# Kernel optimization log

Hardware: AMD Instinct MI355X
Metric: run time of the kernel (lower is better)

## Reference

```python
import jax, jax.numpy as jnp
import numpy as np

D_MODEL = 1024
NUM_HEADS = 16
HEAD_DIM = D_MODEL // NUM_HEADS


def setup_inputs() -> dict:
    key = jax.random.key(0)
    ks = jax.random.split(key, 9)
    B, S, D = 4, 2048, D_MODEL
    scale = 1.0 / np.sqrt(D)
    x = jax.random.normal(ks[0], (B, S, D), dtype=jnp.float32)
    wq = jax.random.normal(ks[1], (D, D), dtype=jnp.float32) * scale
    wk = jax.random.normal(ks[2], (D, D), dtype=jnp.float32) * scale
    wv = jax.random.normal(ks[3], (D, D), dtype=jnp.float32) * scale
    wo = jax.random.normal(ks[4], (D, D), dtype=jnp.float32) * scale
    bq = jax.random.normal(ks[5], (D,), dtype=jnp.float32) * 0.02
    bk = jax.random.normal(ks[6], (D,), dtype=jnp.float32) * 0.02
    bv = jax.random.normal(ks[7], (D,), dtype=jnp.float32) * 0.02
    bo = jax.random.normal(ks[8], (D,), dtype=jnp.float32) * 0.02
    return {"x": x, "wq": wq, "bq": bq, "wk": wk, "bk": bk,
            "wv": wv, "bv": bv, "wo": wo, "bo": bo}


def _split_heads(t):  # [B,S,D] -> [B,H,S,Dh]
    B, S, _ = t.shape
    return t.reshape(B, S, NUM_HEADS, HEAD_DIM).transpose(0, 2, 1, 3)


def reference(x, wq, bq, wk, bk, wv, bv, wo, bo):
    B, S, D = x.shape
    q = _split_heads(x @ wq + bq)  # [B,H,S,Dh]
    k = _split_heads(x @ wk + bk)
    v = _split_heads(x @ wv + bv)
    scores = jnp.einsum("bhqd,bhkd->bhqk", q, k) / jnp.sqrt(
        jnp.asarray(HEAD_DIM, dtype=x.dtype))
    causal = jnp.tril(jnp.ones((S, S), dtype=bool))  # [S,S]
    scores = jnp.where(causal, scores, jnp.finfo(scores.dtype).min)
    attn = jax.nn.softmax(scores, axis=-1)
    ctx = jnp.einsum("bhqk,bhkd->bhqd", attn, v)  # [B,H,S,Dh]
    ctx = ctx.transpose(0, 2, 1, 3).reshape(B, S, D)
    return ctx @ wo + bo
```

## Files before the change

### kernel.cpp

```cpp
#include <hip/hip_runtime.h>
#include <hip/hip_bf16.h>
#include <stdint.h>

#define DMODEL 1024
#define NH 16
#define DH 64
#define BATCH 4
#define SEQ 2048

#if __has_builtin(__builtin_amdgcn_exp2f)
#define EXP2F(x) __builtin_amdgcn_exp2f(x)
#else
#define EXP2F(x) exp2f(x)
#endif

typedef __attribute__((ext_vector_type(8))) short short8;
typedef __attribute__((ext_vector_type(4))) float f32x4;
typedef __attribute__((ext_vector_type(4))) ushort ushort4v;

__device__ __forceinline__ ushort f2bf(float f) {
    union { float f; unsigned u; } v; v.f = f;
    unsigned r = v.u + 0x7fffu + ((v.u >> 16) & 1u);
    return (ushort)(r >> 16);
}

__global__ __launch_bounds__(256) void convert_bf16(const float* __restrict__ src,
                                                    ushort* __restrict__ dst) {
    const size_t i = ((size_t)blockIdx.x * 256 + threadIdx.x) * 8;
    float4 a = *(const float4*)(src + i);
    float4 b = *(const float4*)(src + i + 4);
    short8 r;
    r[0] = (short)f2bf(a.x); r[1] = (short)f2bf(a.y);
    r[2] = (short)f2bf(a.z); r[3] = (short)f2bf(a.w);
    r[4] = (short)f2bf(b.x); r[5] = (short)f2bf(b.y);
    r[6] = (short)f2bf(b.z); r[7] = (short)f2bf(b.w);
    *(short8*)(dst + i) = r;
}

__global__ __launch_bounds__(256) void transpose_cvt_w4(
    const float* __restrict__ s0, const float* __restrict__ s1,
    const float* __restrict__ s2, const float* __restrict__ s3,
    ushort* __restrict__ d0, ushort* __restrict__ d1,
    ushort* __restrict__ d2, ushort* __restrict__ d3) {
    __shared__ ushort tile[64][65];
    const int z = blockIdx.z;
    const float* src = (z == 0) ? s0 : (z == 1) ? s1 : (z == 2) ? s2 : s3;
    ushort* dst = (z == 0) ? d0 : (z == 1) ? d1 : (z == 2) ? d2 : d3;
    const int bx = blockIdx.x * 64;
    const int by = blockIdx.y * 64;
    const int tx = threadIdx.x & 63, ty = threadIdx.x >> 6;
    #pragma unroll
    for (int i = 0; i < 64; i += 4)
        tile[ty + i][tx] = f2bf(src[(size_t)(by + ty + i) * DMODEL + bx + tx]);
    __syncthreads();
    #pragma unroll
    for (int i = 0; i < 64; i += 4)
        dst[(size_t)(bx + ty + i) * DMODEL + by + tx] = tile[tx][ty + i];
}

#define BK 64
#define NT 16

template <int MODE>
__global__ __launch_bounds__(512, 2) void gemm_tile(
    const ushort* __restrict__ A, const ushort* __restrict__ Bt,
    const float* __restrict__ b0, const float* __restrict__ b1,
    const float* __restrict__ b2,
    void* __restrict__ o0v, void* __restrict__ o1v, void* __restrict__ o2v) {
    __shared__ __align__(16) ushort lds[73728];
    const int tid  = threadIdx.x;
    const int lane = tid & 63;
    const int wv   = tid >> 6;

    const int bid = blockIdx.x;
    const int by  = 4 * (bid & 7) + ((bid >> 3) & 3);
    const int bx  = bid >> 5;
    const int mBase = by * 256, nBase = bx * 128;

    const int wm = (wv >> 1) * 64;
    const int wn = (wv & 1) * 64;
    const int frow = lane & 15;
    const int fq   = lane >> 4;
    const int r7   = frow & 7;
    const int sw0  = (fq ^ r7) << 3;
    const int sw1  = ((4 + fq) ^ r7) << 3;

    const int trow = tid >> 3;
    const int tcho = ((tid & 7) ^ (trow & 7)) * 8;
    const ushort* gA = A  + (size_t)(mBase + trow) * DMODEL + tcho;
    const ushort* gB = Bt + (size_t)(nBase + trow) * DMODEL + tcho;
    const int ldsw = wv * 512;

    f32x4 acc[4][4];
    #pragma unroll
    for (int i = 0; i < 4; ++i)
        #pragma unroll
        for (int j = 0; j < 4; ++j) acc[i][j] = (f32x4){0.f, 0.f, 0.f, 0.f};

#define STG(gp, off) __builtin_amdgcn_global_load_lds( \
    (const __attribute__((address_space(1))) void*)(gp), \
    (__attribute__((address_space(3))) void*)&lds[(off) + ldsw], 16, 0, 0)
#define STAGE_A(sb, u, h) STG(gA + (size_t)(h) * 64 * DMODEL + (u) * BK, \
                              (sb) + (h) * 4096)
#define STAGE_B(sb, u, h) STG(gB + (size_t)(h) * 64 * DMODEL + (u) * BK, \
                              (sb) + 16384 + (h) * 4096)

    STAGE_A(0, 0, 0); STAGE_A(0, 0, 1); STAGE_A(0, 0, 2); STAGE_A(0, 0, 3);
    STAGE_B(0, 0, 0); STAGE_B(0, 0, 1);
    STAGE_A(24576, 1, 0); STAGE_A(24576, 1, 1); STAGE_A(24576, 1, 2);
    STAGE_A(24576, 1, 3); STAGE_B(24576, 1, 0); STAGE_B(24576, 1, 1);
    asm volatile("s_waitcnt vmcnt(6)" ::: "memory");
    __builtin_amdgcn_s_barrier();

    int sc = 0;
    #pragma unroll 1
    for (int u = 0; u < NT; ++u) {
        const int scB = sc * 24576;
        const int sp  = (sc == 0) ? 2 : sc - 1;
        const int spB = sp * 24576;
        const ushort* bufA = &lds[scB + wm * 64];
        const ushort* bufB = &lds[scB + 16384 + wn * 64];

        short8 af[4][2], bf[2][2];

        #pragma unroll
        for (int f = 0; f < 4; ++f) {
            const int ro = (f * 16 + frow) * 64;
            af[f][0] = *(const short8*)&bufA[ro + sw0];
            af[f][1] = *(const short8*)&bufA[ro + sw1];
        }
        #pragma unroll
        for (int f2 = 0; f2 < 2; ++f2) {
            const int ro = (f2 * 16 + frow) * 64;
            bf[f2][0] = *(const short8*)&bufB[ro + sw0];
            bf[f2][1] = *(const short8*)&bufB[ro + sw1];
        }
        if (u + 2 < NT) {
            STAGE_A(spB, u + 2, 0); STAGE_A(spB, u + 2, 1); STAGE_A(spB, u + 2, 2);
        }
        __builtin_amdgcn_s_barrier();
        asm volatile("s_waitcnt lgkmcnt(0)" ::: "memory");
        __builtin_amdgcn_s_setprio(1);
        #pragma unroll
        for (int f = 0; f < 4; ++f)
            #pragma unroll
            for (int f2 = 0; f2 < 2; ++f2)
                #pragma unroll
                for (int ks = 0; ks < 2; ++ks)
                    acc[f][f2] = __builtin_amdgcn_mfma_f32_16x16x32_bf16(
                        af[f][ks], bf[f2][ks], acc[f][f2], 0, 0, 0);
        __builtin_amdgcn_s_setprio(0);
        __builtin_amdgcn_s_barrier();

        #pragma unroll
        for (int f2 = 0; f2 < 2; ++f2) {
            const int ro = (32 + f2 * 16 + frow) * 64;
            bf[f2][0] = *(const short8*)&bufB[ro + sw0];
            bf[f2][1] = *(const short8*)&bufB[ro + sw1];
        }
        if (u + 2 < NT) {
            STAGE_A(spB, u + 2, 3); STAGE_B(spB, u + 2, 0); STAGE_B(spB, u + 2, 1);
        }
        __builtin_amdgcn_s_barrier();
        asm volatile("s_waitcnt lgkmcnt(0)" ::: "memory");
        __builtin_amdgcn_s_setprio(1);
        #pragma unroll
        for (int f = 0; f < 4; ++f)
            #pragma unroll
            for (int f2 = 0; f2 < 2; ++f2)
                #pragma unroll
                for (int ks = 0; ks < 2; ++ks)
                    acc[f][2 + f2] = __builtin_amdgcn_mfma_f32_16x16x32_bf16(
                        af[f][ks], bf[f2][ks], acc[f][2 + f2], 0, 0, 0);
        __builtin_amdgcn_s_setprio(0);
        if (u + 2 < NT)       { asm volatile("s_waitcnt vmcnt(6)" ::: "memory"); }
        else if (u + 2 == NT) { asm volatile("s_waitcnt vmcnt(0)" ::: "memory"); }
        __builtin_amdgcn_s_barrier();
        sc = (sc == 2) ? 0 : sc + 1;
    }
#undef STG
#undef STAGE_A
#undef STAGE_B

    const int orow = fq * 4;
    const int ocol = frow;

    if (MODE == 1) {
        #pragma unroll
        for (int i = 0; i < 4; ++i)
            #pragma unroll
            for (int j = 0; j < 4; ++j)
                #pragma unroll
                for (int r = 0; r < 4; ++r) {
                    const int m = mBase + wm + i * 16 + orow + r;
                    const int n = nBase + wn + j * 16 + ocol;
                    ((float*)o0v)[(size_t)m * DMODEL + n] = acc[i][j][r] + b0[n];
                }
        return;
    }

    __syncthreads();
    ushort* o0 = (ushort*)o0v; ushort* o1 = (ushort*)o1v; ushort* o2 = (ushort*)o2v;
    ushort* sw = &lds[wv * 1152];
    const int mat = nBase >> 10;
    const int nb0 = (nBase & 1023) + wn;
    const int hb  = nb0 >> 6;
    const float* bp = (mat == 0) ? b0 : ((mat == 1) ? b1 : b2);
    float bj[4];
    #pragma unroll
    for (int j = 0; j < 4; ++j) bj[j] = bp[nb0 + j * 16 + ocol];
    const int mrow = mBase + wm;
    const int bbq = mrow >> 11;
    const int s0w = mrow & 2047;
    const float qscale = (mat == 0) ? 0.1803368801f : 1.0f;

    if (mat < 2) {
        ushort* obase = ((mat == 0) ? o0 : o1) +
                        ((size_t)(bbq * NH + hb) * SEQ + s0w) * DH;
        const int row = lane >> 2, cc = lane & 3;
        #pragma unroll
        for (int i = 0; i < 4; ++i) {
            #pragma unroll
            for (int j = 0; j < 4; ++j)
                #pragma unroll
                for (int r = 0; r < 4; ++r)
                    sw[(orow + r) * 72 + j * 16 + ocol] =
                        f2bf((acc[i][j][r] + bj[j]) * qscale);
            asm volatile("s_waitcnt lgkmcnt(0)" ::: "memory");
            #pragma unroll
            for (int p = 0; p < 2; ++p) {
                short8 v8 = *(const short8*)&sw[row * 72 + cc * 8 + p * 32];
                *(short8*)&obase[(size_t)(i * 16 + row) * DH + cc * 8 + p * 32] = v8;
            }
            asm volatile("s_waitcnt lgkmcnt(0)" ::: "memory");
        }
    } else {
        const int rowd = lane >> 2, scl = lane & 3;
        #pragma unroll
        for (int j = 0; j < 4; ++j) {
            #pragma unroll
            for (int ii = 0; ii < 4; ++ii)
                #pragma unroll
                for (int r = 0; r < 4; ++r)
                    sw[ocol * 72 + ii * 16 + orow + r] = f2bf(acc[ii][j][r] + bj[j]);
            asm volatile("s_waitcnt lgkmcnt(0)" ::: "memory");
            ushort* vbase = o2 + ((size_t)(bbq * NH + hb) * DH + j * 16 + rowd) * SEQ + s0w;
            #pragma unroll
            for (int p = 0; p < 2; ++p) {
                short8 v8 = *(const short8*)&sw[rowd * 72 + scl * 8 + p * 32];
                *(short8*)&vbase[scl * 8 + p * 32] = v8;
            }
            asm volatile("s_waitcnt lgkmcnt(0)" ::: "memory");
        }
    }
}

#define PSTR 72
__global__ __launch_bounds__(256, 4) void flash_attn(
    const ushort* __restrict__ Q, const ushort* __restrict__ K,
    const ushort* __restrict__ Vt, ushort* __restrict__ ctx) {
    __shared__ __align__(16) ushort Ks[4096];
    __shared__ __align__(16) ushort Vs[4096];
    __shared__ __align__(16) ushort plds[4][16 * PSTR];
    const int lane = threadIdx.x & 63;
    const int wv   = threadIdx.x >> 6;
    const int bh   = blockIdx.x & 63;
    const int Jp   = blockIdx.x >> 6;
    const int bb = bh >> 4, h = bh & 15;

    const ushort* Qb = Q + (size_t)bh * SEQ * DH;
    const ushort* Kb = K + (size_t)bh * SEQ * DH;
    const ushort* Vb = Vt + (size_t)bh * DH * SEQ;

    const int frow = lane & 15;
    const int fq   = lane >> 4;
    const int r7s  = lane >> 3;
    const int csw  = (lane & 7) ^ r7s;

    short8 ones;
    #pragma unroll
    for (int i = 0; i < 8; ++i) ones[i] = (short)0x3F80;

    #pragma unroll 1
    for (int half = 0; half < 2; ++half) {
        const int Je = half ? (31 - Jp) : Jp;
        const int q0 = Je * 64 + wv * 16;
        const int qmax = q0 + 15;

        short8 qf[2];
        #pragma unroll
        for (int ks = 0; ks < 2; ++ks)
            qf[ks] = *(const short8*)&Qb[(size_t)(q0 + frow) * DH + ks * 32 + fq * 8];

        f32x4 o[4], lacc;
        #pragma unroll
        for (int t = 0; t < 4; ++t) o[t] = (f32x4){0.f, 0.f, 0.f, 0.f};
        lacc = (f32x4){0.f, 0.f, 0.f, 0.f};

        #pragma unroll 1
        for (int it = 0; it <= Je; ++it) {
            const int k0 = it * 64;
            __syncthreads();
            #pragma unroll
            for (int i = 0; i < 2; ++i) {
                const int c = wv * 2 + i;
                const ushort* gk = Kb + (size_t)(k0 + c * 8 + r7s) * DH + csw * 8;
                __builtin_amdgcn_global_load_lds(
                    (const __attribute__((address_space(1))) void*)gk,
                    (__attribute__((address_space(3))) void*)&Ks[c * 512], 16, 0, 0);
                const ushort* gv = Vb + (size_t)(c * 8 + r7s) * SEQ + k0 + csw * 8;
                __builtin_amdgcn_global_load_lds(
                    (const __attribute__((address_space(1))) void*)gv,
                    (__attribute__((address_space(3))) void*)&Vs[c * 512], 16, 0, 0);
            }
            __syncthreads();

            if (it < Je) {
                f32x4 sacc[4];
                #pragma unroll
                for (int nt = 0; nt < 4; ++nt) sacc[nt] = (f32x4){0.f, 0.f, 0.f, 0.f};
                #pragma unroll
                for (int nt = 0; nt < 4; ++nt) {
                    const int row = nt * 16 + frow, r7 = row & 7;
                    #pragma unroll
                    for (int ks = 0; ks < 2; ++ks) {
                        short8 kf = *(const short8*)
                            &Ks[(row >> 3) * 512 + r7 * 64 + (((ks * 4 + fq) ^ r7) * 8)];
                        sacc[nt] = __builtin_amdgcn_mfma_f32_16x16x32_bf16(kf, qf[ks],
                                                                          sacc[nt], 0, 0, 0);
                    }
                }
                #pragma unroll
                for (int nt = 0; nt < 4; ++nt) {
                    float p0 = EXP2F(sacc[nt][0]);
                    float p1 = EXP2F(sacc[nt][1]);
                    float p2 = EXP2F(sacc[nt][2]);
                    float p3 = EXP2F(sacc[nt][3]);
                    uint2 dw;
                    dw.x = __builtin_amdgcn_perm(__float_as_uint(p1), __float_as_uint(p0),
                                                 0x07060302u);
                    dw.y = __builtin_amdgcn_perm(__float_as_uint(p3), __float_as_uint(p2),
                                                 0x07060302u);
                    *(uint2*)&plds[wv][frow * PSTR + nt * 16 + fq * 4] = dw;
                }
                asm volatile("s_waitcnt lgkmcnt(0)" ::: "memory");
                #pragma unroll
                for (int kc = 0; kc < 2; ++kc) {
                    short8 pf = *(const short8*)&plds[wv][frow * PSTR + kc * 32 + fq * 8];
                    lacc = __builtin_amdgcn_mfma_f32_16x16x32_bf16(ones, pf, lacc, 0, 0, 0);
                    #pragma unroll
                    for (int t = 0; t < 4; ++t) {
                        const int row = t * 16 + frow, r7 = row & 7;
                        short8 vf = *(const short8*)
                            &Vs[(row >> 3) * 512 + r7 * 64 + (((kc * 4 + fq) ^ r7) * 8)];
                        o[t] = __builtin_amdgcn_mfma_f32_16x16x32_bf16(vf, pf, o[t], 0, 0, 0);
                    }
                }
            } else {
                const int qrow = q0 + frow;
                f32x4 sacc[4];
                #pragma unroll
                for (int nt = 0; nt < 4; ++nt) sacc[nt] = (f32x4){0.f, 0.f, 0.f, 0.f};
                #pragma unroll
                for (int nt = 0; nt < 4; ++nt)
                    if (k0 + nt * 16 <= qmax) {
                        const int row = nt * 16 + frow, r7 = row & 7;
                        #pragma unroll
                        for (int ks = 0; ks < 2; ++ks) {
                            short8 kf = *(const short8*)
                                &Ks[(row >> 3) * 512 + r7 * 64 + (((ks * 4 + fq) ^ r7) * 8)];
                            sacc[nt] = __builtin_amdgcn_mfma_f32_16x16x32_bf16(kf, qf[ks],
                                                                              sacc[nt], 0, 0, 0);
                        }
                    }
                #pragma unroll
                for (int nt = 0; nt < 4; ++nt) {
                    uint2 dw; dw.x = 0u; dw.y = 0u;
                    if (k0 + nt * 16 <= qmax) {
                        float pp[4];
                        #pragma unroll
                        for (int r = 0; r < 4; ++r) {
                            const float e = EXP2F(sacc[nt][r]);
                            pp[r] = (k0 + nt * 16 + fq * 4 + r <= qrow) ? e : 0.f;
                        }
                        dw.x = __builtin_amdgcn_perm(__float_as_uint(pp[1]),
                                                     __float_as_uint(pp[0]), 0x07060302u);
                        dw.y = __builtin_amdgcn_perm(__float_as_uint(pp[3]),
                                                     __float_as_uint(pp[2]), 0x07060302u);
                    }
                    *(uint2*)&plds[wv][frow * PSTR + nt * 16 + fq * 4] = dw;
                }
                asm volatile("s_waitcnt lgkmcnt(0)" ::: "memory");
                #pragma unroll
                for (int kc = 0; kc < 2; ++kc) {
                    if (k0 + kc * 32 <= qmax) {
                        short8 pf = *(const short8*)&plds[wv][frow * PSTR + kc * 32 + fq * 8];
                        lacc = __builtin_amdgcn_mfma_f32_16x16x32_bf16(ones, pf, lacc, 0, 0, 0);
                        #pragma unroll
                        for (int t = 0; t < 4; ++t) {
                            const int row = t * 16 + frow, r7 = row & 7;
                            short8 vf = *(const short8*)
                                &Vs[(row >> 3) * 512 + r7 * 64 + (((kc * 4 + fq) ^ r7) * 8)];
                            o[t] = __builtin_amdgcn_mfma_f32_16x16x32_bf16(vf, pf, o[t], 0, 0, 0);
                        }
                    }
                }
            }
        }
        const float inv = 1.0f / lacc[0];
        const int qrow = q0 + frow;
        ushort* cp = ctx + (size_t)(bb * SEQ + qrow) * DMODEL + h * DH;
        #pragma unroll
        for (int t = 0; t < 4; ++t) {
            ushort4v ov;
            #pragma unroll
            for (int r = 0; r < 4; ++r) ov[r] = f2bf(o[t][r] * inv);
            *(ushort4v*)&cp[t * 16 + fq * 4] = ov;
        }
    }
}

extern "C" void kernel_launch(void* const* d_in, const int* in_sizes, int n_in,
                              void* d_out, int out_size, void* d_ws, size_t ws_size,
                              hipStream_t stream) {
    const float* x  = (const float*)d_in[0];
    const float* wq = (const float*)d_in[1];
    const float* bq = (const float*)d_in[2];
    const float* wk = (const float*)d_in[3];
    const float* bk = (const float*)d_in[4];
    const float* wvp = (const float*)d_in[5];
    const float* bv = (const float*)d_in[6];
    const float* wo = (const float*)d_in[7];
    const float* bo = (const float*)d_in[8];
    float* out = (float*)d_out;
    ushort* ws = (ushort*)d_ws;

    const size_t QSZ = (size_t)BATCH * NH * SEQ * DH;
    ushort* xbf   = ws;
    ushort* qws   = ws + QSZ;
    ushort* kws   = ws + 2 * QSZ;
    ushort* vtws  = ws + 3 * QSZ;
    ushort* ctxws = ws + 4 * QSZ;
    ushort* wtqkv = ws + 5 * QSZ;
    ushort* wto   = wtqkv + 3 * (size_t)DMODEL * DMODEL;

    dim3 tb(256);
    convert_bf16<<<dim3(4096), tb, 0, stream>>>(x, xbf);
    transpose_cvt_w4<<<dim3(16, 16, 4), tb, 0, stream>>>(
        wq, wk, wvp, wo,
        wtqkv, wtqkv + (size_t)DMODEL * DMODEL, wtqkv + 2 * (size_t)DMODEL * DMODEL, wto);

    gemm_tile<0><<<dim3(768), dim3(512), 0, stream>>>(xbf, wtqkv, bq, bk, bv,
                                                      qws, kws, vtws);
    flash_attn<<<dim3(1024), tb, 0, stream>>>(qws, kws, vtws, ctxws);
    gemm_tile<1><<<dim3(256), dim3(512), 0, stream>>>(ctxws, wto, bo, nullptr, nullptr,
                                                      out, nullptr, nullptr);
}
```

Before: 242.5 us.

## Double-buffer K/V tiles in flash attention with 128-row query blocks

The attention kernel now uses 512-thread blocks covering 128 query rows, with two K/V LDS buffers, so the next tile's global-to-LDS copy is issued before computing on the current one. This replaces the two per-iteration syncthreads with one waitcnt plus barrier. It also raises wave priority around the PV MFMAs. Each K/V tile is shared by twice as many waves, which should cut global traffic per query row. The cost is more LDS per block, and on diagonal tiles half the waves sit idle.

```diff
diff --git a/kernel.cpp b/kernel.cpp
--- a/kernel.cpp
+++ b/kernel.cpp
@@ -256,14 +256,15 @@
 }
 
 #define PSTR 72
-__global__ __launch_bounds__(256, 4) void flash_attn(
+__global__ __launch_bounds__(512, 6) void flash_attn(
     const ushort* __restrict__ Q, const ushort* __restrict__ K,
     const ushort* __restrict__ Vt, ushort* __restrict__ ctx) {
-    __shared__ __align__(16) ushort Ks[4096];
-    __shared__ __align__(16) ushort Vs[4096];
-    __shared__ __align__(16) ushort plds[4][16 * PSTR];
-    const int lane = threadIdx.x & 63;
-    const int wv   = threadIdx.x >> 6;
+    __shared__ __align__(16) ushort Ks[2][4096];
+    __shared__ __align__(16) ushort Vs[2][4096];
+    __shared__ __align__(16) ushort plds[8][16 * PSTR];
+    const int tid  = threadIdx.x;
+    const int lane = tid & 63;
+    const int wv   = tid >> 6;
     const int bh   = blockIdx.x & 63;
     const int Jp   = blockIdx.x >> 6;
     const int bb = bh >> 4, h = bh & 15;
@@ -274,17 +275,23 @@
 
     const int frow = lane & 15;
     const int fq   = lane >> 4;
-    const int r7s  = lane >> 3;
-    const int csw  = (lane & 7) ^ r7s;
+    const int trow = tid >> 3;
+    const int tcho = ((tid & 7) ^ (trow & 7)) * 8;
+    const int ldsw = wv * 512;
 
     short8 ones;
     #pragma unroll
     for (int i = 0; i < 8; ++i) ones[i] = (short)0x3F80;
 
+#define FA_STG(gp, lp) __builtin_amdgcn_global_load_lds( \
+    (const __attribute__((address_space(1))) void*)(gp), \
+    (__attribute__((address_space(3))) void*)(lp), 16, 0, 0)
+
     #pragma unroll 1
     for (int half = 0; half < 2; ++half) {
-        const int Je = half ? (31 - Jp) : Jp;
-        const int q0 = Je * 64 + wv * 16;
+        const int J = half ? (15 - Jp) : Jp;
+        const int ktmax = 2 * J + 1;
+        const int q0 = J * 128 + (wv >> 2) * 64 + (wv & 3) * 16;
         const int qmax = q0 + 15;
 
         short8 qf[2];
@@ -297,25 +304,25 @@
         for (int t = 0; t < 4; ++t) o[t] = (f32x4){0.f, 0.f, 0.f, 0.f};
         lacc = (f32x4){0.f, 0.f, 0.f, 0.f};
 
+        FA_STG(Kb + (size_t)trow * DH + tcho, &Ks[0][ldsw]);
+        FA_STG(Vb + (size_t)trow * SEQ + tcho, &Vs[0][ldsw]);
+        asm volatile("s_waitcnt vmcnt(0)" ::: "memory");
+        __builtin_amdgcn_s_barrier();
+
         #pragma unroll 1
-        for (int it = 0; it <= Je; ++it) {
-            const int k0 = it * 64;
-            __syncthreads();
-            #pragma unroll
-            for (int i = 0; i < 2; ++i) {
-                const int c = wv * 2 + i;
-                const ushort* gk = Kb + (size_t)(k0 + c * 8 + r7s) * DH + csw * 8;
-                __builtin_amdgcn_global_load_lds(
-                    (const __attribute__((address_space(1))) void*)gk,
-                    (__attribute__((address_space(3))) void*)&Ks[c * 512], 16, 0, 0);
-                const ushort* gv = Vb + (size_t)(c * 8 + r7s) * SEQ + k0 + csw * 8;
-                __builtin_amdgcn_global_load_lds(
-                    (const __attribute__((address_space(1))) void*)gv,
-                    (__attribute__((address_space(3))) void*)&Vs[c * 512], 16, 0, 0);
+        for (int kt = 0; kt <= ktmax; ++kt) {
+            const int k0 = kt * 64;
+            const int cur = kt & 1;
+            if (kt < ktmax) {
+                const int kn = k0 + 64;
+                FA_STG(Kb + (size_t)(kn + trow) * DH + tcho, &Ks[cur ^ 1][ldsw]);
+                FA_STG(Vb + (size_t)trow * SEQ + kn + tcho, &Vs[cur ^ 1][ldsw]);
             }
-            __syncthreads();
-
-            if (it < Je) {
+            const ushort* Ksc = Ks[cur];
+            const ushort* Vsc = Vs[cur];
+
+            if (k0 <= qmax) {
+            if (k0 + 64 <= q0) {
                 f32x4 sacc[4];
                 #pragma unroll
                 for (int nt = 0; nt < 4; ++nt) sacc[nt] = (f32x4){0.f, 0.f, 0.f, 0.f};
@@ -325,7 +332,7 @@
                     #pragma unroll
                     for (int ks = 0; ks < 2; ++ks) {
                         short8 kf = *(const short8*)
-                            &Ks[(row >> 3) * 512 + r7 * 64 + (((ks * 4 + fq) ^ r7) * 8)];
+                            &Ksc[(row >> 3) * 512 + r7 * 64 + (((ks * 4 + fq) ^ r7) * 8)];
                         sacc[nt] = __builtin_amdgcn_mfma_f32_16x16x32_bf16(kf, qf[ks],
                                                                           sacc[nt], 0, 0, 0);
                     }
@@ -348,13 +355,15 @@
                 for (int kc = 0; kc < 2; ++kc) {
                     short8 pf = *(const short8*)&plds[wv][frow * PSTR + kc * 32 + fq * 8];
                     lacc = __builtin_amdgcn_mfma_f32_16x16x32_bf16(ones, pf, lacc, 0, 0, 0);
+                    __builtin_amdgcn_s_setprio(1);
                     #pragma unroll
                     for (int t = 0; t < 4; ++t) {
                         const int row = t * 16 + frow, r7 = row & 7;
                         short8 vf = *(const short8*)
-                            &Vs[(row >> 3) * 512 + r7 * 64 + (((kc * 4 + fq) ^ r7) * 8)];
+                            &Vsc[(row >> 3) * 512 + r7 * 64 + (((kc * 4 + fq) ^ r7) * 8)];
                         o[t] = __builtin_amdgcn_mfma_f32_16x16x32_bf16(vf, pf, o[t], 0, 0, 0);
                     }
+                    __builtin_amdgcn_s_setprio(0);
                 }
             } else {
                 const int qrow = q0 + frow;
@@ -368,7 +377,7 @@
                         #pragma unroll
                         for (int ks = 0; ks < 2; ++ks) {
                             short8 kf = *(const short8*)
-                                &Ks[(row >> 3) * 512 + r7 * 64 + (((ks * 4 + fq) ^ r7) * 8)];
+                                &Ksc[(row >> 3) * 512 + r7 * 64 + (((ks * 4 + fq) ^ r7) * 8)];
                             sacc[nt] = __builtin_amdgcn_mfma_f32_16x16x32_bf16(kf, qf[ks],
                                                                               sacc[nt], 0, 0, 0);
                         }
@@ -400,13 +409,18 @@
                         for (int t = 0; t < 4; ++t) {
                             const int row = t * 16 + frow, r7 = row & 7;
                             short8 vf = *(const short8*)
-                                &Vs[(row >> 3) * 512 + r7 * 64 + (((kc * 4 + fq) ^ r7) * 8)];
+                                &Vsc[(row >> 3) * 512 + r7 * 64 + (((kc * 4 + fq) ^ r7) * 8)];
                             o[t] = __builtin_amdgcn_mfma_f32_16x16x32_bf16(vf, pf, o[t], 0, 0, 0);
                         }
                     }
                 }
             }
-        }
+            }
+
+            asm volatile("s_waitcnt lgkmcnt(0) vmcnt(0)" ::: "memory");
+            __builtin_amdgcn_s_barrier();
+        }
+
         const float inv = 1.0f / lacc[0];
         const int qrow = q0 + frow;
         ushort* cp = ctx + (size_t)(bb * SEQ + qrow) * DMODEL + h * DH;
@@ -418,6 +432,7 @@
             *(ushort4v*)&cp[t * 16 + fq * 4] = ov;
         }
     }
+#undef FA_STG
 }
 
 extern "C" void kernel_launch(void* const* d_in, const int* in_sizes, int n_in,
@@ -452,7 +467,7 @@
 
     gemm_tile<0><<<dim3(768), dim3(512), 0, stream>>>(xbf, wtqkv, bq, bk, bv,
                                                       qws, kws, vtws);
-    flash_attn<<<dim3(1024), tb, 0, stream>>>(qws, kws, vtws, ctxws);
+    flash_attn<<<dim3(512), dim3(512), 0, stream>>>(qws, kws, vtws, ctxws);
     gemm_tile<1><<<dim3(256), dim3(512), 0, stream>>>(ctxws, wto, bo, nullptr, nullptr,
                                                       out, nullptr, nullptr);
 }
```

Result: faster. 232.9 us (-4.0%).
